# Kernel tuning notes

Hardware: AMD Instinct MI355X
Metric: run time of the kernel (lower is better)

## Reference

```python
import jax, jax.numpy as jnp
import numpy as np

B, N, RESC, LAT, UNIT = 8, 32, 256.0, 1536, 512
CHS = [64, 64, 128, 256, 512, 512]
HS = [128, 64, 32, 16, 8, 1]


def _align(feat, P):
    # torch F.grid_sample(feat, 2*P.unsqueeze(-2)/RESC - 1, 'bilinear', 'border', align_corners=False).squeeze(-1)
    # feat: [B,C,H,W], P: [B,M,2] (x,y) pixel coords in [0,RESC); returns [B,C,M]
    Bn, C, H, W = feat.shape
    gx = 2.0 * P[..., 0] / RESC - 1.0
    gy = 2.0 * P[..., 1] / RESC - 1.0
    # align_corners=False unnormalize, then border clamp
    x = jnp.clip(((gx + 1.0) * W - 1.0) * 0.5, 0.0, W - 1.0)
    y = jnp.clip(((gy + 1.0) * H - 1.0) * 0.5, 0.0, H - 1.0)
    x0 = jnp.floor(x); y0 = jnp.floor(y)
    wx = (x - x0)[:, None, :]; wy = (y - y0)[:, None, :]
    x0i = x0.astype(jnp.int32); y0i = y0.astype(jnp.int32)
    x1i = jnp.minimum(x0i + 1, W - 1); y1i = jnp.minimum(y0i + 1, H - 1)
    flat = feat.reshape(Bn, C, H * W)
    def gat(yi, xi):
        return jnp.take_along_axis(flat, (yi * W + xi)[:, None, :], axis=2)  # [B,C,M]
    v00 = gat(y0i, x0i); v01 = gat(y0i, x1i); v10 = gat(y1i, x0i); v11 = gat(y1i, x1i)
    return v00 * (1 - wx) * (1 - wy) + v01 * wx * (1 - wy) + v10 * (1 - wx) * wy + v11 * wx * wy


def _conv1(x, w, b):
    # 1x1 Conv1d: [B,Cin,M] x [Cout,Cin] -> [B,Cout,M]
    return jnp.einsum('bci,oc->boi', x, w) + b[None, :, None]


def _rescls(x, p):
    # ResCls(n=1): intro -> (relu(BN) -> chorus, residual) -> outro ; BN in eval mode
    iw, ib, bg, bb, bm, bv, cw, cb, ow, ob = p
    x = _conv1(x, iw, ib)
    d = jax.nn.relu((x - bm[None, :, None]) * (bg / jnp.sqrt(bv + 1e-5))[None, :, None] + bb[None, :, None])
    x = x + _conv1(d, cw, cb)
    return _conv1(x, ow, ob)


def _forward(feats, P, n, gp, pp):
    # node features: concat of per-level aligned features  [B, LAT, N]
    F_ = jnp.concatenate([_align(f, P) for f in feats], axis=1)
    # edge midpoints ep[b, i*N+j] = (P[i] + P[j]) / 2  -> [B, N*N, 2]
    ep = ((P[:, :, None, :] + P[:, None, :, :]) * 0.5).reshape(B, N * N, 2)
    # L: first LAT channels = F[:, :, i], next LAT channels = F[:, :, j]
    Fi = jnp.broadcast_to(F_[:, :, :, None], (B, LAT, N, N)).reshape(B, LAT, N * N)
    Fj = jnp.broadcast_to(F_[:, :, None, :], (B, LAT, N, N)).reshape(B, LAT, N * N)
    E = jnp.concatenate([_align(f, ep) for f in feats], axis=1)  # [B, LAT, N*N]
    CE = jnp.concatenate([Fi, Fj, E], axis=1)  # [B, 3*LAT, N*N]
    gate = jax.nn.sigmoid(_rescls(CE, gp))  # [B, 1, N*N]
    pr = _rescls(CE, pp)  # [B, 64, N*N]
    pr = pr / jnp.maximum(jnp.linalg.norm(pr, axis=1, keepdims=True), 1e-12)  # F.normalize(dim=1)
    m = jnp.arange(N) < n[:, None]  # [B, N]
    mask = (m[:, None, :] & m[:, :, None]).reshape(B, 1, N * N).astype(CE.dtype)
    return (gate * pr * mask).reshape(B, 64, N, N)


def setup_inputs() -> dict:
    key = jax.random.key(0)
    ks = jax.random.split(key, 20)
    d = {}
    for i, (c, h) in enumerate(zip(CHS, HS)):
        d[f'feat{i}'] = jax.random.normal(ks[i], (B, c, h, h), jnp.float32)
    d['P'] = jax.random.uniform(ks[6], (B, N, 2), jnp.float32) * RESC
    d['n'] = jax.random.randint(ks[7], (B,), 16, N + 1, jnp.int32)
    def w(k, shape):
        return jax.random.normal(k, shape, jnp.float32) * 0.02
    for pre, cout, k0 in (('g', 1, 8), ('p', 64, 12)):
        d[pre + '_iw'] = w(ks[k0], (UNIT, 3 * LAT)); d[pre + '_ib'] = jnp.zeros((UNIT,), jnp.float32)
        d[pre + '_bg'] = jnp.ones((UNIT,), jnp.float32); d[pre + '_bb'] = jnp.zeros((UNIT,), jnp.float32)
        d[pre + '_bm'] = jnp.zeros((UNIT,), jnp.float32)
        d[pre + '_bv'] = jax.random.uniform(ks[k0 + 1], (UNIT,), jnp.float32) + 0.5
        d[pre + '_cw'] = w(ks[k0 + 2], (UNIT, UNIT)); d[pre + '_cb'] = jnp.zeros((UNIT,), jnp.float32)
        d[pre + '_ow'] = w(ks[k0 + 3], (cout, UNIT)); d[pre + '_ob'] = jnp.zeros((cout,), jnp.float32)
    return d


def reference(feat0, feat1, feat2, feat3, feat4, feat5, P, n,
              g_iw, g_ib, g_bg, g_bb, g_bm, g_bv, g_cw, g_cb, g_ow, g_ob,
              p_iw, p_ib, p_bg, p_bb, p_bm, p_bv, p_cw, p_cb, p_ow, p_ob):
    feats = (feat0, feat1, feat2, feat3, feat4, feat5)
    gp = (g_iw, g_ib, g_bg, g_bb, g_bm, g_bv, g_cw, g_cb, g_ow, g_ob)
    pp = (p_iw, p_ib, p_bg, p_bb, p_bm, p_bv, p_cw, p_cb, p_ow, p_ob)
    return _forward(feats, P, n, gp, pp)
```

## Files before the change

### kernel.cpp

```cpp
#include <hip/hip_runtime.h>
#include <hip/hip_bf16.h>

using bf16 = __hip_bfloat16;
using short8 = __attribute__((ext_vector_type(8))) short;
using f32x4  = __attribute__((ext_vector_type(4))) float;
typedef unsigned int u32;

#define LAT_ 1536

__device__ __forceinline__ void glds16(const bf16* g, bf16* l) {
  __builtin_amdgcn_global_load_lds(
      (const __attribute__((address_space(1))) void*)g,
      (__attribute__((address_space(3))) void*)l, 16, 0, 0);
}
__device__ __forceinline__ float b2f(bf16 x) { return __bfloat162float(x); }
__device__ __forceinline__ bf16 f2b(float x) { return __float2bfloat16(x); }

template<int C, int W>
__device__ __forceinline__ void trans_tile(const float* __restrict__ src, bf16* __restrict__ dst,
                                           int b, int hw0, int c0, bf16 (*tile)[72], int t) {
  constexpr int HW = W * W;
  {
    int cl = t >> 2, h0 = (t & 3) * 16;
    const float* sp = src + (long)(b * C + c0 + cl) * HW + hw0 + h0;
    #pragma unroll
    for (int k = 0; k < 16; k += 4) {
      float4 v = *(const float4*)(sp + k);
      tile[h0 + k + 0][cl] = f2b(v.x);
      tile[h0 + k + 1][cl] = f2b(v.y);
      tile[h0 + k + 2][cl] = f2b(v.z);
      tile[h0 + k + 3][cl] = f2b(v.w);
    }
  }
  __syncthreads();
  {
    int hwl = t >> 2, cc = (t & 3) * 16;
    bf16* dp = dst + ((long)b * HW + hw0 + hwl) * C + c0 + cc;
    #pragma unroll
    for (int k = 0; k < 16; k += 2) {
      __hip_bfloat162 pr;
      pr.x = tile[hwl][cc + k];
      pr.y = tile[hwl][cc + k + 1];
      *(__hip_bfloat162*)(dp + k) = pr;
    }
  }
}

__global__ __launch_bounds__(256) void prep_k(
    const float* __restrict__ g_iw, const float* __restrict__ p_iw,
    const float* __restrict__ p_cw, const float* __restrict__ p_ow, const float* __restrict__ f5,
    const float* __restrict__ g_bg, const float* __restrict__ g_bb, const float* __restrict__ g_bm,
    const float* __restrict__ g_bv, const float* __restrict__ p_bg, const float* __restrict__ p_bb,
    const float* __restrict__ p_bm, const float* __restrict__ p_bv,
    const float* __restrict__ g_ib, const float* __restrict__ p_ib, const float* __restrict__ p_cb,
    const float* __restrict__ g_ow, const float* __restrict__ g_cw,
    const float* __restrict__ f0, const float* __restrict__ f1, const float* __restrict__ f2,
    const float* __restrict__ f3, const float* __restrict__ f4,
    bf16* __restrict__ Wp, bf16* __restrict__ pcw16, bf16* __restrict__ pow16,
    bf16* __restrict__ T5, float* __restrict__ bnp, float* __restrict__ u,
    bf16* __restrict__ T0, bf16* __restrict__ T1, bf16* __restrict__ T2,
    bf16* __restrict__ T3, bf16* __restrict__ T4) {
  __shared__ bf16 tile[64][72];
  __shared__ float ured[4][64];
  int B = blockIdx.x, t = threadIdx.x;
  if (B < 18432) {
    int seg = B / 3072;
    int idx = (B % 3072) * 256 + t;
    if (idx < 512 * 1536) {
      int r = idx / 1536, c = idx % 1536;
      const float* src; int co;
      switch (seg) {
        case 0: src = g_iw; co = 0;    break;
        case 1: src = g_iw; co = 1536; break;
        case 2: src = p_iw; co = 0;    break;
        case 3: src = p_iw; co = 1536; break;
        case 4: src = g_iw; co = 3072; break;
        default: src = p_iw; co = 3072; break;
      }
      Wp[(long)seg * 512 * 1536 + idx] = f2b(src[(long)r * 4608 + co + c]);
    }
    return;
  }
  if (B < 19456) { int idx = (B - 18432) * 256 + t; pcw16[idx] = f2b(p_cw[idx]); return; }
  if (B < 19584) { int idx = (B - 19456) * 256 + t; pow16[idx] = f2b(p_ow[idx]); return; }
  if (B < 19600) { int idx = (B - 19584) * 256 + t; T5[idx] = f2b(f5[idx]); return; }
  if (B < 19602) {
    int k = (B - 19600) * 256 + t;
    if (k < 512) {
      float sg = g_bg[k] / sqrtf(g_bv[k] + 1e-5f);
      bnp[k] = sg; bnp[512 + k] = g_bb[k] - g_bm[k] * sg;
      float sp = p_bg[k] / sqrtf(p_bv[k] + 1e-5f);
      bnp[1024 + k] = sp; bnp[1536 + k] = p_bb[k] - p_bm[k] * sp;
      bnp[2048 + k] = g_ib[k]; bnp[2560 + k] = p_ib[k];
      bnp[3584 + k] = p_cb[k];
    }
    return;
  }
  if (B < 19610) {
    int k0 = (B - 19602) * 64;
    int kk = t & 63, part = t >> 6;
    int k = k0 + kk;
    float s = 0.f;
    for (int o = part * 128; o < part * 128 + 128; ++o)
      s = fmaf(g_ow[o], g_cw[o * 512 + k], s);
    ured[part][kk] = s;
    __syncthreads();
    if (part == 0) u[k] = ured[0][kk] + ured[1][kk] + ured[2][kk] + ured[3][kk];
    return;
  }
  {
    int q = B - 19610;
    int b = q / 376, tt = q % 376;
    if (tt < 256)      trans_tile<64, 128>(f0, T0, b, tt * 64, 0, tile, t);
    else if (tt < 320) trans_tile<64, 64 >(f1, T1, b, (tt - 256) * 64, 0, tile, t);
    else if (tt < 352) { int z = tt - 320; trans_tile<128, 32>(f2, T2, b, (z & 15) * 64, (z >> 4) * 64, tile, t); }
    else if (tt < 368) { int z = tt - 352; trans_tile<256, 16>(f3, T3, b, (z & 3) * 64, (z >> 2) * 64, tile, t); }
    else               { int z = tt - 368; trans_tile<512, 8 >(f4, T4, b, 0, z * 64, tile, t); }
  }
}

__device__ __forceinline__ float blo(u32 r) { return __uint_as_float(r << 16); }
__device__ __forceinline__ float bhi(u32 r) { return __uint_as_float(r & 0xffff0000u); }

template<int C, int W>
__device__ __forceinline__ void proc2(const bf16* __restrict__ T, int b,
    const float* MX, const float* MY, bf16* __restrict__ Sb, int koff, int t) {
  constexpr int C2 = C / 2, HW = W * W;
  const bf16* Tb = T + (long)b * HW * C;
  for (int idx = t; idx < 16 * C2; idx += 256) {
    int q = idx / C2, c2 = idx % C2;
    float x = MX[q], y = MY[q];
    float fx = fminf(fmaxf(x * ((float)W / 256.f) - 0.5f, 0.f), (float)(W - 1));
    float fy = fminf(fmaxf(y * ((float)W / 256.f) - 0.5f, 0.f), (float)(W - 1));
    float x0f = floorf(fx), y0f = floorf(fy);
    float wx = fx - x0f, wy = fy - y0f;
    int x0 = (int)x0f, y0 = (int)y0f;
    int x1 = min(x0 + 1, W - 1), y1 = min(y0 + 1, W - 1);
    u32 r00 = *(const u32*)&Tb[(y0 * W + x0) * C + 2 * c2];
    u32 r01 = *(const u32*)&Tb[(y0 * W + x1) * C + 2 * c2];
    u32 r10 = *(const u32*)&Tb[(y1 * W + x0) * C + 2 * c2];
    u32 r11 = *(const u32*)&Tb[(y1 * W + x1) * C + 2 * c2];
    float w00 = (1.f - wx) * (1.f - wy), w01 = wx * (1.f - wy);
    float w10 = (1.f - wx) * wy,        w11 = wx * wy;
    float vlo = blo(r00) * w00 + blo(r01) * w01 + blo(r10) * w10 + blo(r11) * w11;
    float vhi = bhi(r00) * w00 + bhi(r01) * w01 + bhi(r10) * w10 + bhi(r11) * w11;
    __hip_bfloat162 pr;
    pr.x = f2b(vlo); pr.y = f2b(vhi);
    *(__hip_bfloat162*)&Sb[(long)q * LAT_ + koff + 2 * c2] = pr;
  }
}

__global__ __launch_bounds__(256) void sample5_k(
    const bf16* __restrict__ T0, const bf16* __restrict__ T1, const bf16* __restrict__ T2,
    const bf16* __restrict__ T3, const bf16* __restrict__ T4, const bf16* __restrict__ T5,
    const float* __restrict__ P, bf16* __restrict__ Sball) {
  int b = blockIdx.z, p0 = blockIdx.x * 16, lvl = blockIdx.y, t = threadIdx.x;
  __shared__ float Px[32], Py[32], MX[16], MY[16];
  if (t < 32) { Px[t] = P[(b * 32 + t) * 2]; Py[t] = P[(b * 32 + t) * 2 + 1]; }
  __syncthreads();
  if (t < 16) {
    int m = p0 + t;
    float x, y;
    if (m < 32) { x = Px[m]; y = Py[m]; }
    else { int ij = m - 32, i = ij >> 5, j = ij & 31;
           x = 0.5f * (Px[i] + Px[j]); y = 0.5f * (Py[i] + Py[j]); }
    MX[t] = x; MY[t] = y;
  }
  __syncthreads();
  bf16* Sb = Sball + ((long)b * 1056 + p0) * LAT_;
  switch (lvl) {
    case 0: proc2<64, 128>(T0, b, MX, MY, Sb, 0,    t); break;
    case 1: proc2<64, 64 >(T1, b, MX, MY, Sb, 64,   t); break;
    case 2: proc2<128, 32>(T2, b, MX, MY, Sb, 128,  t); break;
    case 3: proc2<256, 16>(T3, b, MX, MY, Sb, 256,  t); break;
    case 4: proc2<512, 8 >(T4, b, MX, MY, Sb, 512,  t); break;
    default:
      for (int idx = t; idx < 16 * 256; idx += 256) {
        int q = idx >> 8, c2 = idx & 255;
        *(__hip_bfloat162*)&Sb[(long)q * LAT_ + 1024 + 2 * c2] =
            *(const __hip_bfloat162*)&T5[b * 512 + 2 * c2];
      }
  }
}

__global__ __launch_bounds__(256) void nodegemm_k(
    const bf16* __restrict__ Sball, const bf16* __restrict__ Wp, float* __restrict__ A4) {
  int b = blockIdx.y;
  int n0 = blockIdx.x * 64;
  int t = threadIdx.x, w = t >> 6, lane = t & 63;
  int nn = n0 + w * 16;
  int frow = lane & 15, fko = (lane >> 4) * 8;
  const bf16* Ab = Sball + (long)b * 1056 * LAT_;
  f32x4 acc[2] = {};
  for (int kb = 0; kb < LAT_; kb += 32) {
    short8 bq = *(const short8*)&Wp[(long)(nn + frow) * LAT_ + kb + fko];
    #pragma unroll
    for (int i = 0; i < 2; ++i) {
      short8 aq = *(const short8*)&Ab[(long)(i * 16 + frow) * LAT_ + kb + fko];
      acc[i] = __builtin_amdgcn_mfma_f32_16x16x32_bf16(aq, bq, acc[i], 0, 0, 0);
    }
  }
  #pragma unroll
  for (int i = 0; i < 2; ++i)
    #pragma unroll
    for (int r = 0; r < 4; ++r) {
      int m = i * 16 + (lane >> 4) * 4 + r;
      int n = nn + (lane & 15);
      A4[(long)b * 65536 + m * 2048 + n] = acc[i][r];
    }
}

__global__ __launch_bounds__(256) void edge_k(
    const bf16* __restrict__ Sball, const bf16* __restrict__ WpE,
    const float* __restrict__ bnp, const float* __restrict__ A4,
    bf16* __restrict__ XFh, bf16* __restrict__ DH) {
  int b = blockIdx.z;
  int m0 = blockIdx.x * 128, n0 = blockIdx.y * 128;
  const bf16* A = Sball + (long)b * 1056 * LAT_ + 32 * LAT_;
  __shared__ bf16 Ash[128 * 32];
  __shared__ bf16 Bsh[128 * 32];
  int t = threadIdx.x, w = t >> 6, lane = t & 63;
  int mh = (w & 1) * 64, nh = (w >> 1) * 64;
  int frow = lane & 15, cf = lane >> 4;
  int lrow = lane >> 2, lchunk = lane & 3;
  int csw = (lrow >> 1) & 3;
  int sA = (cf ^ ((frow >> 1) & 3)) * 8;
  f32x4 acc[4][4] = {};
  for (int kb = 0; kb < LAT_; kb += 32) {
    #pragma unroll
    for (int q = 0; q < 2; ++q) {
      int ra = q * 64 + w * 16 + lrow;
      glds16(&A[(long)(m0 + ra) * LAT_ + kb + (lchunk ^ csw) * 8],   &Ash[ra * 32 + lchunk * 8]);
      glds16(&WpE[(long)(n0 + ra) * LAT_ + kb + (lchunk ^ csw) * 8], &Bsh[ra * 32 + lchunk * 8]);
    }
    __syncthreads();
    short8 af[4], bq[4];
    #pragma unroll
    for (int i = 0; i < 4; ++i) af[i] = *(const short8*)&Ash[(mh + i * 16 + frow) * 32 + sA];
    #pragma unroll
    for (int j = 0; j < 4; ++j) bq[j] = *(const short8*)&Bsh[(nh + j * 16 + frow) * 32 + sA];
    #pragma unroll
    for (int i = 0; i < 4; ++i)
      #pragma unroll
      for (int j = 0; j < 4; ++j)
        acc[i][j] = __builtin_amdgcn_mfma_f32_16x16x32_bf16(af[i], bq[j], acc[i][j], 0, 0, 0);
    __syncthreads();
  }
  #pragma unroll
  for (int i = 0; i < 4; ++i) {
    #pragma unroll
    for (int j = 0; j < 4; ++j) {
      #pragma unroll
      for (int r = 0; r < 4; ++r) {
        int m = m0 + mh + i * 16 + (lane >> 4) * 4 + r;
        int n = n0 + nh + j * 16 + (lane & 15);
        int nt = n >> 9, nn2 = n & 511;
        float v = acc[i][j][r] + bnp[2048 + n]
                + A4[((long)b * 32 + (m >> 5)) * 2048 + nt * 1024 + nn2]
                + A4[((long)b * 32 + (m & 31)) * 2048 + nt * 1024 + 512 + nn2];
        XFh[((long)b * 1024 + m) * 1024 + n] = f2b(v);
        float d = fmaxf(fmaf(v, bnp[nt * 1024 + nn2], bnp[nt * 1024 + 512 + nn2]), 0.f);
        DH[((long)b * 1024 + m) * 1024 + n] = f2b(d);
      }
    }
  }
}

__global__ __launch_bounds__(256) void chorus_k(
    const bf16* __restrict__ DH, const bf16* __restrict__ pcw16,
    const float* __restrict__ bnp, const bf16* __restrict__ XFh,
    bf16* __restrict__ Yp16) {
  int b = blockIdx.z;
  int m0 = blockIdx.x * 128, n0 = blockIdx.y * 128;
  const bf16* A = DH + (long)b * 1024 * 1024 + 512;
  __shared__ bf16 Ash[128 * 32];
  __shared__ bf16 Bsh[128 * 32];
  int t = threadIdx.x, w = t >> 6, lane = t & 63;
  int mh = (w & 1) * 64, nh = (w >> 1) * 64;
  int frow = lane & 15, cf = lane >> 4;
  int lrow = lane >> 2, lchunk = lane & 3;
  int csw = (lrow >> 1) & 3;
  int sA = (cf ^ ((frow >> 1) & 3)) * 8;
  f32x4 acc[4][4] = {};
  for (int kb = 0; kb < 512; kb += 32) {
    #pragma unroll
    for (int q = 0; q < 2; ++q) {
      int ra = q * 64 + w * 16 + lrow;
      glds16(&A[(long)(m0 + ra) * 1024 + kb + (lchunk ^ csw) * 8],    &Ash[ra * 32 + lchunk * 8]);
      glds16(&pcw16[(long)(n0 + ra) * 512 + kb + (lchunk ^ csw) * 8], &Bsh[ra * 32 + lchunk * 8]);
    }
    __syncthreads();
    short8 af[4], bq[4];
    #pragma unroll
    for (int i = 0; i < 4; ++i) af[i] = *(const short8*)&Ash[(mh + i * 16 + frow) * 32 + sA];
    #pragma unroll
    for (int j = 0; j < 4; ++j) bq[j] = *(const short8*)&Bsh[(nh + j * 16 + frow) * 32 + sA];
    #pragma unroll
    for (int i = 0; i < 4; ++i)
      #pragma unroll
      for (int j = 0; j < 4; ++j)
        acc[i][j] = __builtin_amdgcn_mfma_f32_16x16x32_bf16(af[i], bq[j], acc[i][j], 0, 0, 0);
    __syncthreads();
  }
  #pragma unroll
  for (int i = 0; i < 4; ++i)
    #pragma unroll
    for (int j = 0; j < 4; ++j)
      #pragma unroll
      for (int r = 0; r < 4; ++r) {
        int m = m0 + mh + i * 16 + (lane >> 4) * 4 + r;
        int n = n0 + nh + j * 16 + (lane & 15);
        float v = acc[i][j][r] + bnp[3584 + n]
                + b2f(XFh[((long)b * 1024 + m) * 1024 + 512 + n]);
        Yp16[((long)b * 1024 + m) * 512 + n] = f2b(v);
      }
}

__global__ __launch_bounds__(256) void outro_k(
    const bf16* __restrict__ Yp16, const bf16* __restrict__ pow16,
    const float* __restrict__ p_ob, float* __restrict__ PR) {
  int b = blockIdx.z;
  const bf16* Ab = Yp16 + (long)b * 1024 * 512;
  int m0 = blockIdx.x * 64;
  __shared__ bf16 Ash[64][40];
  __shared__ bf16 Bsh[64][40];
  int t = threadIdx.x, w = t >> 6, lane = t & 63;
  int mq = w * 16;
  int frow = lane & 15, fko = (lane >> 4) * 8;
  f32x4 acc[4] = {};
  for (int kb = 0; kb < 512; kb += 32) {
    { int r = t >> 2, ko = (t & 3) * 8;
      *(uint4*)&Ash[r][ko] = *(const uint4*)&Ab[(long)(m0 + r) * 512 + kb + ko];
      *(uint4*)&Bsh[r][ko] = *(const uint4*)&pow16[(long)r * 512 + kb + ko]; }
    __syncthreads();
    short8 af = *(const short8*)&Ash[mq + frow][fko];
    #pragma unroll
    for (int j = 0; j < 4; ++j) {
      short8 bq = *(const short8*)&Bsh[j * 16 + frow][fko];
      acc[j] = __builtin_amdgcn_mfma_f32_16x16x32_bf16(af, bq, acc[j], 0, 0, 0);
    }
    __syncthreads();
  }
  #pragma unroll
  for (int j = 0; j < 4; ++j)
    #pragma unroll
    for (int r = 0; r < 4; ++r) {
      int m = m0 + mq + (lane >> 4) * 4 + r;
      int n = j * 16 + (lane & 15);
      PR[((long)b * 1024 + m) * 64 + n] = acc[j][r] + p_ob[n];
    }
}

__global__ __launch_bounds__(256) void final3_k(
    const bf16* __restrict__ XFh, const bf16* __restrict__ DH, const float* __restrict__ PR,
    const float* __restrict__ u, const float* __restrict__ g_ow,
    const float* __restrict__ g_cb, const float* __restrict__ g_ob,
    const int* __restrict__ n, float* __restrict__ out) {
  int gw = blockIdx.x * 4 + (threadIdx.x >> 6);
  int lane = threadIdx.x & 63;
  int b = gw >> 10, ij = gw & 1023;
  const bf16* xr = XFh + ((long)b * 1024 + ij) * 1024;
  const bf16* dr = DH  + ((long)b * 1024 + ij) * 1024;
  float gl = 0.f;
  #pragma unroll
  for (int q = 0; q < 8; ++q) {
    int nn = q * 64 + lane;
    gl = fmaf(g_ow[nn], b2f(xr[nn]) + g_cb[nn], gl);
    gl = fmaf(u[nn], b2f(dr[nn]), gl);
  }
  #pragma unroll
  for (int off = 32; off; off >>= 1) gl += __shfl_down(gl, off);
  gl = __shfl(gl, 0) + g_ob[0];
  float gate = 1.f / (1.f + expf(-gl));
  int i = ij >> 5, j = ij & 31, nb = n[b];
  float maskv = (i < nb && j < nb) ? 1.f : 0.f;
  float v = PR[((long)b * 1024 + ij) * 64 + lane];
  float ss = v * v;
  #pragma unroll
  for (int off = 32; off; off >>= 1) ss += __shfl_down(ss, off);
  ss = __shfl(ss, 0);
  float scale = gate * maskv / fmaxf(sqrtf(ss), 1e-12f);
  out[((long)b * 64 + lane) * 1024 + ij] = v * scale;
}

extern "C" void kernel_launch(void* const* d_in, const int* in_sizes, int n_in,
                              void* d_out, int out_size, void* d_ws, size_t ws_size,
                              hipStream_t stream) {
  const float* f0 = (const float*)d_in[0];
  const float* f1 = (const float*)d_in[1];
  const float* f2 = (const float*)d_in[2];
  const float* f3 = (const float*)d_in[3];
  const float* f4 = (const float*)d_in[4];
  const float* f5 = (const float*)d_in[5];
  const float* P  = (const float*)d_in[6];
  const int*   n  = (const int*)d_in[7];
  const float *g_iw=(const float*)d_in[8],  *g_ib=(const float*)d_in[9],
              *g_bg=(const float*)d_in[10], *g_bb=(const float*)d_in[11],
              *g_bm=(const float*)d_in[12], *g_bv=(const float*)d_in[13],
              *g_cw=(const float*)d_in[14], *g_cb=(const float*)d_in[15],
              *g_ow=(const float*)d_in[16], *g_ob=(const float*)d_in[17];
  const float *p_iw=(const float*)d_in[18], *p_ib=(const float*)d_in[19],
              *p_bg=(const float*)d_in[20], *p_bb=(const float*)d_in[21],
              *p_bm=(const float*)d_in[22], *p_bv=(const float*)d_in[23],
              *p_cw=(const float*)d_in[24], *p_cb=(const float*)d_in[25],
              *p_ow=(const float*)d_in[26], *p_ob=(const float*)d_in[27];
  float* out = (float*)d_out;
  char* wsb = (char*)d_ws;

  bf16*  Sb    = (bf16*)(wsb + 0);
  bf16*  Wp    = (bf16*)(wsb + 25952256);
  bf16*  pcw16 = (bf16*)(wsb + 35389440);
  bf16*  pow16 = (bf16*)(wsb + 35913728);
  bf16*  T5    = (bf16*)(wsb + 35979264);
  float* bnp   = (float*)(wsb + 35987456);
  float* u     = (float*)(wsb + 36003840);
  float* A4    = (float*)(wsb + 36005888);
  bf16*  XFh   = (bf16*)(wsb + 38103040);
  bf16*  DH    = (bf16*)(wsb + 54880256);
  bf16*  Yp16  = (bf16*)(wsb + 71657472);
  float* PR    = (float*)(wsb + 80046080);
  bf16*  T0 = (bf16*)(wsb + 38103040);
  bf16*  T1 = (bf16*)(wsb + 54880256);
  bf16*  T2 = (bf16*)(wsb + 59074560);
  bf16*  T3 = (bf16*)(wsb + 61171712);
  bf16*  T4 = (bf16*)(wsb + 62220288);
  bf16*  WpE = Wp + (long)2048 * LAT_;

  prep_k<<<22618, 256, 0, stream>>>(g_iw, p_iw, p_cw, p_ow, f5,
      g_bg, g_bb, g_bm, g_bv, p_bg, p_bb, p_bm, p_bv, g_ib, p_ib, p_cb,
      g_ow, g_cw, f0, f1, f2, f3, f4,
      Wp, pcw16, pow16, T5, bnp, u, T0, T1, T2, T3, T4);
  sample5_k<<<dim3(66, 6, 8), 256, 0, stream>>>(T0, T1, T2, T3, T4, T5, P, Sb);
  nodegemm_k<<<dim3(32, 8), 256, 0, stream>>>(Sb, Wp, A4);
  edge_k<<<dim3(8, 8, 8), 256, 0, stream>>>(Sb, WpE, bnp, A4, XFh, DH);
  chorus_k<<<dim3(8, 4, 8), 256, 0, stream>>>(DH, pcw16, bnp, XFh, Yp16);
  outro_k<<<dim3(16, 1, 8), 256, 0, stream>>>(Yp16, pow16, p_ob, PR);
  final3_k<<<2048, 256, 0, stream>>>(XFh, DH, PR, u, g_ow, g_cb, g_ob, n, out);
}
```

Measured before the change: 265.3 us.

## Fuse gate reduction into edge GEMM epilogue and merge outro with final normalize

```diff
diff --git a/kernel.cpp b/kernel.cpp
--- a/kernel.cpp
+++ b/kernel.cpp
@@ -54,14 +54,16 @@
     const float* __restrict__ p_bm, const float* __restrict__ p_bv,
     const float* __restrict__ g_ib, const float* __restrict__ p_ib, const float* __restrict__ p_cb,
     const float* __restrict__ g_ow, const float* __restrict__ g_cw,
+    const float* __restrict__ g_cb, const float* __restrict__ g_ob,
     const float* __restrict__ f0, const float* __restrict__ f1, const float* __restrict__ f2,
     const float* __restrict__ f3, const float* __restrict__ f4,
     bf16* __restrict__ Wp, bf16* __restrict__ pcw16, bf16* __restrict__ pow16,
     bf16* __restrict__ T5, float* __restrict__ bnp, float* __restrict__ u,
+    float* __restrict__ gacc,
     bf16* __restrict__ T0, bf16* __restrict__ T1, bf16* __restrict__ T2,
     bf16* __restrict__ T3, bf16* __restrict__ T4) {
   __shared__ bf16 tile[64][72];
-  __shared__ float ured[4][64];
+  __shared__ float red[256];
   int B = blockIdx.x, t = threadIdx.x;
   if (B < 18432) {
     int seg = B / 3072;
@@ -97,6 +99,7 @@
     return;
   }
   if (B < 19610) {
+    __shared__ float ured[4][64];
     int k0 = (B - 19602) * 64;
     int kk = t & 63, part = t >> 6;
     int k = k0 + kk;
@@ -108,8 +111,19 @@
     if (part == 0) u[k] = ured[0][kk] + ured[1][kk] + ured[2][kk] + ured[3][kk];
     return;
   }
+  if (B == 19610) {
+    red[t] = g_ow[t] * g_cb[t] + g_ow[t + 256] * g_cb[t + 256];
+    __syncthreads();
+    for (int off = 128; off; off >>= 1) {
+      if (t < off) red[t] += red[t + off];
+      __syncthreads();
+    }
+    if (t == 0) bnp[3072] = red[0] + g_ob[0];
+    return;
+  }
+  if (B < 19643) { int idx = (B - 19611) * 256 + t; gacc[idx] = 0.f; return; }
   {
-    int q = B - 19610;
+    int q = B - 19643;
     int b = q / 376, tt = q % 376;
     if (tt < 256)      trans_tile<64, 128>(f0, T0, b, tt * 64, 0, tile, t);
     else if (tt < 320) trans_tile<64, 64 >(f1, T1, b, (tt - 256) * 64, 0, tile, t);
@@ -213,7 +227,8 @@
 __global__ __launch_bounds__(256) void edge_k(
     const bf16* __restrict__ Sball, const bf16* __restrict__ WpE,
     const float* __restrict__ bnp, const float* __restrict__ A4,
-    bf16* __restrict__ XFh, bf16* __restrict__ DH) {
+    const float* __restrict__ u, const float* __restrict__ g_ow,
+    bf16* __restrict__ XFh, bf16* __restrict__ DH, float* __restrict__ gacc) {
   int b = blockIdx.z;
   int m0 = blockIdx.x * 128, n0 = blockIdx.y * 128;
   const bf16* A = Sball + (long)b * 1056 * LAT_ + 32 * LAT_;
@@ -221,24 +236,22 @@
   __shared__ bf16 Bsh[128 * 32];
   int t = threadIdx.x, w = t >> 6, lane = t & 63;
   int mh = (w & 1) * 64, nh = (w >> 1) * 64;
-  int frow = lane & 15, cf = lane >> 4;
+  int frow = lane & 15, fko = (lane >> 4) * 8;
   int lrow = lane >> 2, lchunk = lane & 3;
-  int csw = (lrow >> 1) & 3;
-  int sA = (cf ^ ((frow >> 1) & 3)) * 8;
   f32x4 acc[4][4] = {};
   for (int kb = 0; kb < LAT_; kb += 32) {
     #pragma unroll
     for (int q = 0; q < 2; ++q) {
       int ra = q * 64 + w * 16 + lrow;
-      glds16(&A[(long)(m0 + ra) * LAT_ + kb + (lchunk ^ csw) * 8],   &Ash[ra * 32 + lchunk * 8]);
-      glds16(&WpE[(long)(n0 + ra) * LAT_ + kb + (lchunk ^ csw) * 8], &Bsh[ra * 32 + lchunk * 8]);
+      glds16(&A[(long)(m0 + ra) * LAT_ + kb + lchunk * 8],   &Ash[ra * 32 + lchunk * 8]);
+      glds16(&WpE[(long)(n0 + ra) * LAT_ + kb + lchunk * 8], &Bsh[ra * 32 + lchunk * 8]);
     }
     __syncthreads();
     short8 af[4], bq[4];
     #pragma unroll
-    for (int i = 0; i < 4; ++i) af[i] = *(const short8*)&Ash[(mh + i * 16 + frow) * 32 + sA];
-    #pragma unroll
-    for (int j = 0; j < 4; ++j) bq[j] = *(const short8*)&Bsh[(nh + j * 16 + frow) * 32 + sA];
+    for (int i = 0; i < 4; ++i) af[i] = *(const short8*)&Ash[(mh + i * 16 + frow) * 32 + fko];
+    #pragma unroll
+    for (int j = 0; j < 4; ++j) bq[j] = *(const short8*)&Bsh[(nh + j * 16 + frow) * 32 + fko];
     #pragma unroll
     for (int i = 0; i < 4; ++i)
       #pragma unroll
@@ -246,21 +259,62 @@
         acc[i][j] = __builtin_amdgcn_mfma_f32_16x16x32_bf16(af[i], bq[j], acc[i][j], 0, 0, 0);
     __syncthreads();
   }
-  #pragma unroll
-  for (int i = 0; i < 4; ++i) {
-    #pragma unroll
-    for (int j = 0; j < 4; ++j) {
+  if (n0 < 512) {
+    float pg[16];
+    #pragma unroll
+    for (int z = 0; z < 16; ++z) pg[z] = 0.f;
+    #pragma unroll
+    for (int i = 0; i < 4; ++i) {
       #pragma unroll
-      for (int r = 0; r < 4; ++r) {
-        int m = m0 + mh + i * 16 + (lane >> 4) * 4 + r;
+      for (int j = 0; j < 4; ++j) {
         int n = n0 + nh + j * 16 + (lane & 15);
-        int nt = n >> 9, nn2 = n & 511;
-        float v = acc[i][j][r] + bnp[2048 + n]
-                + A4[((long)b * 32 + (m >> 5)) * 2048 + nt * 1024 + nn2]
-                + A4[((long)b * 32 + (m & 31)) * 2048 + nt * 1024 + 512 + nn2];
-        XFh[((long)b * 1024 + m) * 1024 + n] = f2b(v);
-        float d = fmaxf(fmaf(v, bnp[nt * 1024 + nn2], bnp[nt * 1024 + 512 + nn2]), 0.f);
-        DH[((long)b * 1024 + m) * 1024 + n] = f2b(d);
+        float gw = g_ow[n], uu = u[n];
+        float sc = bnp[n], sh = bnp[512 + n], ib = bnp[2048 + n];
+        #pragma unroll
+        for (int r = 0; r < 4; ++r) {
+          int m = m0 + mh + i * 16 + (lane >> 4) * 4 + r;
+          float v = acc[i][j][r] + ib
+                  + A4[((long)b * 32 + (m >> 5)) * 2048 + n]
+                  + A4[((long)b * 32 + (m & 31)) * 2048 + 512 + n];
+          float d = fmaxf(fmaf(v, sc, sh), 0.f);
+          pg[i * 4 + r] += gw * v + uu * d;
+        }
+      }
+    }
+    #pragma unroll
+    for (int z = 0; z < 16; ++z) {
+      float v = pg[z];
+      v += __shfl_xor(v, 1, 16);
+      v += __shfl_xor(v, 2, 16);
+      v += __shfl_xor(v, 4, 16);
+      v += __shfl_xor(v, 8, 16);
+      pg[z] = v;
+    }
+    if ((lane & 15) == 0) {
+      #pragma unroll
+      for (int z = 0; z < 16; ++z) {
+        int m = m0 + mh + (z >> 2) * 16 + (lane >> 4) * 4 + (z & 3);
+        atomicAdd(&gacc[(long)b * 1024 + m], pg[z]);
+      }
+    }
+  } else {
+    #pragma unroll
+    for (int i = 0; i < 4; ++i) {
+      #pragma unroll
+      for (int j = 0; j < 4; ++j) {
+        int n = n0 + nh + j * 16 + (lane & 15);
+        int np = n - 512;
+        float sc = bnp[1024 + np], sh = bnp[1536 + np], ib = bnp[2048 + n];
+        #pragma unroll
+        for (int r = 0; r < 4; ++r) {
+          int m = m0 + mh + i * 16 + (lane >> 4) * 4 + r;
+          float v = acc[i][j][r] + ib
+                  + A4[((long)b * 32 + (m >> 5)) * 2048 + 1024 + np]
+                  + A4[((long)b * 32 + (m & 31)) * 2048 + 1536 + np];
+          long e = ((long)b * 1024 + m) * 512 + np;
+          XFh[e] = f2b(v);
+          DH[e]  = f2b(fmaxf(fmaf(v, sc, sh), 0.f));
+        }
       }
     }
   }
@@ -272,29 +326,27 @@
     bf16* __restrict__ Yp16) {
   int b = blockIdx.z;
   int m0 = blockIdx.x * 128, n0 = blockIdx.y * 128;
-  const bf16* A = DH + (long)b * 1024 * 1024 + 512;
+  const bf16* A = DH + (long)b * 1024 * 512;
   __shared__ bf16 Ash[128 * 32];
   __shared__ bf16 Bsh[128 * 32];
   int t = threadIdx.x, w = t >> 6, lane = t & 63;
   int mh = (w & 1) * 64, nh = (w >> 1) * 64;
-  int frow = lane & 15, cf = lane >> 4;
+  int frow = lane & 15, fko = (lane >> 4) * 8;
   int lrow = lane >> 2, lchunk = lane & 3;
-  int csw = (lrow >> 1) & 3;
-  int sA = (cf ^ ((frow >> 1) & 3)) * 8;
   f32x4 acc[4][4] = {};
   for (int kb = 0; kb < 512; kb += 32) {
     #pragma unroll
     for (int q = 0; q < 2; ++q) {
       int ra = q * 64 + w * 16 + lrow;
-      glds16(&A[(long)(m0 + ra) * 1024 + kb + (lchunk ^ csw) * 8],    &Ash[ra * 32 + lchunk * 8]);
-      glds16(&pcw16[(long)(n0 + ra) * 512 + kb + (lchunk ^ csw) * 8], &Bsh[ra * 32 + lchunk * 8]);
+      glds16(&A[(long)(m0 + ra) * 512 + kb + lchunk * 8],      &Ash[ra * 32 + lchunk * 8]);
+      glds16(&pcw16[(long)(n0 + ra) * 512 + kb + lchunk * 8],  &Bsh[ra * 32 + lchunk * 8]);
     }
     __syncthreads();
     short8 af[4], bq[4];
     #pragma unroll
-    for (int i = 0; i < 4; ++i) af[i] = *(const short8*)&Ash[(mh + i * 16 + frow) * 32 + sA];
-    #pragma unroll
-    for (int j = 0; j < 4; ++j) bq[j] = *(const short8*)&Bsh[(nh + j * 16 + frow) * 32 + sA];
+    for (int i = 0; i < 4; ++i) af[i] = *(const short8*)&Ash[(mh + i * 16 + frow) * 32 + fko];
+    #pragma unroll
+    for (int j = 0; j < 4; ++j) bq[j] = *(const short8*)&Bsh[(nh + j * 16 + frow) * 32 + fko];
     #pragma unroll
     for (int i = 0; i < 4; ++i)
       #pragma unroll
@@ -311,19 +363,22 @@
         int m = m0 + mh + i * 16 + (lane >> 4) * 4 + r;
         int n = n0 + nh + j * 16 + (lane & 15);
         float v = acc[i][j][r] + bnp[3584 + n]
-                + b2f(XFh[((long)b * 1024 + m) * 1024 + 512 + n]);
+                + b2f(XFh[((long)b * 1024 + m) * 512 + n]);
         Yp16[((long)b * 1024 + m) * 512 + n] = f2b(v);
       }
 }
 
-__global__ __launch_bounds__(256) void outro_k(
+__global__ __launch_bounds__(256) void ofinal_k(
     const bf16* __restrict__ Yp16, const bf16* __restrict__ pow16,
-    const float* __restrict__ p_ob, float* __restrict__ PR) {
-  int b = blockIdx.z;
+    const float* __restrict__ p_ob, const float* __restrict__ gacc,
+    const float* __restrict__ bnp, const int* __restrict__ nvec,
+    float* __restrict__ out) {
+  int b = blockIdx.y;
+  int m0 = blockIdx.x * 64;
   const bf16* Ab = Yp16 + (long)b * 1024 * 512;
-  int m0 = blockIdx.x * 64;
   __shared__ bf16 Ash[64][40];
   __shared__ bf16 Bsh[64][40];
+  __shared__ float ol[64][65];
   int t = threadIdx.x, w = t >> 6, lane = t & 63;
   int mq = w * 16;
   int frow = lane & 15, fko = (lane >> 4) * 8;
@@ -341,46 +396,57 @@
     }
     __syncthreads();
   }
+  float pr[4][4], ssl[4] = {0.f, 0.f, 0.f, 0.f};
+  #pragma unroll
+  for (int j = 0; j < 4; ++j) {
+    float bias = p_ob[j * 16 + (lane & 15)];
+    #pragma unroll
+    for (int r = 0; r < 4; ++r) {
+      float v = acc[j][r] + bias;
+      pr[j][r] = v;
+      ssl[r] = fmaf(v, v, ssl[r]);
+    }
+  }
+  #pragma unroll
+  for (int r = 0; r < 4; ++r) {
+    float v = ssl[r];
+    v += __shfl_xor(v, 1, 16);
+    v += __shfl_xor(v, 2, 16);
+    v += __shfl_xor(v, 4, 16);
+    v += __shfl_xor(v, 8, 16);
+    ssl[r] = v;
+  }
+  int nb = nvec[b];
+  float gconst = bnp[3072];
+  float scale[4];
+  #pragma unroll
+  for (int r = 0; r < 4; ++r) {
+    int m = m0 + mq + (lane >> 4) * 4 + r;
+    float gl = gacc[(long)b * 1024 + m] + gconst;
+    float gate = 1.f / (1.f + expf(-gl));
+    int ii = m >> 5, jj = m & 31;
+    float maskv = (ii < nb && jj < nb) ? 1.f : 0.f;
+    scale[r] = gate * maskv / fmaxf(sqrtf(ssl[r]), 1e-12f);
+  }
   #pragma unroll
   for (int j = 0; j < 4; ++j)
     #pragma unroll
-    for (int r = 0; r < 4; ++r) {
-      int m = m0 + mq + (lane >> 4) * 4 + r;
-      int n = j * 16 + (lane & 15);
-      PR[((long)b * 1024 + m) * 64 + n] = acc[j][r] + p_ob[n];
-    }
-}
-
-__global__ __launch_bounds__(256) void final3_k(
-    const bf16* __restrict__ XFh, const bf16* __restrict__ DH, const float* __restrict__ PR,
-    const float* __restrict__ u, const float* __restrict__ g_ow,
-    const float* __restrict__ g_cb, const float* __restrict__ g_ob,
-    const int* __restrict__ n, float* __restrict__ out) {
-  int gw = blockIdx.x * 4 + (threadIdx.x >> 6);
-  int lane = threadIdx.x & 63;
-  int b = gw >> 10, ij = gw & 1023;
-  const bf16* xr = XFh + ((long)b * 1024 + ij) * 1024;
-  const bf16* dr = DH  + ((long)b * 1024 + ij) * 1024;
-  float gl = 0.f;
-  #pragma unroll
-  for (int q = 0; q < 8; ++q) {
-    int nn = q * 64 + lane;
-    gl = fmaf(g_ow[nn], b2f(xr[nn]) + g_cb[nn], gl);
-    gl = fmaf(u[nn], b2f(dr[nn]), gl);
-  }
-  #pragma unroll
-  for (int off = 32; off; off >>= 1) gl += __shfl_down(gl, off);
-  gl = __shfl(gl, 0) + g_ob[0];
-  float gate = 1.f / (1.f + expf(-gl));
-  int i = ij >> 5, j = ij & 31, nb = n[b];
-  float maskv = (i < nb && j < nb) ? 1.f : 0.f;
-  float v = PR[((long)b * 1024 + ij) * 64 + lane];
-  float ss = v * v;
-  #pragma unroll
-  for (int off = 32; off; off >>= 1) ss += __shfl_down(ss, off);
-  ss = __shfl(ss, 0);
-  float scale = gate * maskv / fmaxf(sqrtf(ss), 1e-12f);
-  out[((long)b * 64 + lane) * 1024 + ij] = v * scale;
+    for (int r = 0; r < 4; ++r)
+      ol[mq + (lane >> 4) * 4 + r][j * 16 + (lane & 15)] = pr[j][r] * scale[r];
+  __syncthreads();
+  {
+    int c = t >> 2, ms = (t & 3) * 16;
+    float* op = out + ((long)b * 64 + c) * 1024 + m0 + ms;
+    #pragma unroll
+    for (int k = 0; k < 16; k += 4) {
+      float4 v;
+      v.x = ol[ms + k + 0][c];
+      v.y = ol[ms + k + 1][c];
+      v.z = ol[ms + k + 2][c];
+      v.w = ol[ms + k + 3][c];
+      *(float4*)(op + k) = v;
+    }
+  }
 }
 
 extern "C" void kernel_launch(void* const* d_in, const int* in_sizes, int n_in,
@@ -414,26 +480,25 @@
   bf16*  T5    = (bf16*)(wsb + 35979264);
   float* bnp   = (float*)(wsb + 35987456);
   float* u     = (float*)(wsb + 36003840);
-  float* A4    = (float*)(wsb + 36005888);
-  bf16*  XFh   = (bf16*)(wsb + 38103040);
-  bf16*  DH    = (bf16*)(wsb + 54880256);
-  bf16*  Yp16  = (bf16*)(wsb + 71657472);
-  float* PR    = (float*)(wsb + 80046080);
-  bf16*  T0 = (bf16*)(wsb + 38103040);
-  bf16*  T1 = (bf16*)(wsb + 54880256);
-  bf16*  T2 = (bf16*)(wsb + 59074560);
-  bf16*  T3 = (bf16*)(wsb + 61171712);
-  bf16*  T4 = (bf16*)(wsb + 62220288);
+  float* gacc  = (float*)(wsb + 36005888);
+  float* A4    = (float*)(wsb + 36038656);
+  bf16*  XFh   = (bf16*)(wsb + 38135808);
+  bf16*  DH    = (bf16*)(wsb + 46524416);
+  bf16*  Yp16  = (bf16*)(wsb + 54913024);
+  bf16*  T0 = (bf16*)(wsb + 38135808);
+  bf16*  T1 = (bf16*)(wsb + 54913024);
+  bf16*  T2 = (bf16*)(wsb + 59107328);
+  bf16*  T3 = (bf16*)(wsb + 61204480);
+  bf16*  T4 = (bf16*)(wsb + 62253056);
   bf16*  WpE = Wp + (long)2048 * LAT_;
 
-  prep_k<<<22618, 256, 0, stream>>>(g_iw, p_iw, p_cw, p_ow, f5,
+  prep_k<<<22651, 256, 0, stream>>>(g_iw, p_iw, p_cw, p_ow, f5,
       g_bg, g_bb, g_bm, g_bv, p_bg, p_bb, p_bm, p_bv, g_ib, p_ib, p_cb,
-      g_ow, g_cw, f0, f1, f2, f3, f4,
-      Wp, pcw16, pow16, T5, bnp, u, T0, T1, T2, T3, T4);
+      g_ow, g_cw, g_cb, g_ob, f0, f1, f2, f3, f4,
+      Wp, pcw16, pow16, T5, bnp, u, gacc, T0, T1, T2, T3, T4);
   sample5_k<<<dim3(66, 6, 8), 256, 0, stream>>>(T0, T1, T2, T3, T4, T5, P, Sb);
   nodegemm_k<<<dim3(32, 8), 256, 0, stream>>>(Sb, Wp, A4);
-  edge_k<<<dim3(8, 8, 8), 256, 0, stream>>>(Sb, WpE, bnp, A4, XFh, DH);
+  edge_k<<<dim3(8, 8, 8), 256, 0, stream>>>(Sb, WpE, bnp, A4, u, g_ow, XFh, DH, gacc);
   chorus_k<<<dim3(8, 4, 8), 256, 0, stream>>>(DH, pcw16, bnp, XFh, Yp16);
-  outro_k<<<dim3(16, 1, 8), 256, 0, stream>>>(Yp16, pow16, p_ob, PR);
-  final3_k<<<2048, 256, 0, stream>>>(XFh, DH, PR, u, g_ow, g_cb, g_ob, n, out);
-}
+  ofinal_k<<<dim3(16, 8), 256, 0, stream>>>(Yp16, pow16, p_ob, gacc, bnp, n, out);
+}
```

New measurement: 256.8 us. 1.03x faster.
